# Kernel tuning notes

Hardware: AMD Instinct MI355X
Metric: run time of the kernel (lower is better)

The kernel has to match this reference:

```python
import jax, jax.numpy as jnp
import numpy as np

N, D, B, H = 131072, 512, 512, 8  # nodes, hidden_dim, graphs, heads


def setup_inputs() -> dict:
    key = jax.random.key(0)
    ks = jax.random.split(key, 4)
    x = jax.random.normal(ks[0], (N, D), jnp.float32)
    # sorted segment ids; every graph nonempty (matches torch batch.max()+1 semantics)
    batch = jnp.sort(jnp.arange(N, dtype=jnp.int32) % B)
    query = jax.random.normal(ks[1], (D,), jnp.float32)          # nn.Parameter(randn(1,1,D))
    W_in = jax.random.normal(ks[2], (3 * D, D), jnp.float32) / np.sqrt(D)  # MHA in_proj_weight
    b_in = jnp.zeros((3 * D,), jnp.float32)
    W_out = jax.random.normal(ks[3], (D, D), jnp.float32) / np.sqrt(D)     # MHA out_proj
    b_out = jnp.zeros((D,), jnp.float32)
    return {"x": x, "batch": batch, "num_graphs": B, "query": query,
            "W_in": W_in, "b_in": b_in, "W_out": W_out, "b_out": b_out}


def reference(x, batch, num_graphs, query, W_in, b_in, W_out, b_out):
    # Fused ragged single-query multihead attention pooling (eval mode: dropout off).
    D = x.shape[1]
    dh = D // H
    scale = 1.0 / np.sqrt(dh)
    # q/k/v projections (torch MHA packed in_proj: rows [0:D]=q, [D:2D]=k, [2D:3D]=v)
    q = ((query @ W_in[:D].T + b_in[:D]) * scale).reshape(H, dh)       # [H, dh], shared across graphs
    k = (x @ W_in[D:2 * D].T + b_in[D:2 * D]).reshape(-1, H, dh)       # [N, H, dh]
    v = (x @ W_in[2 * D:].T + b_in[2 * D:]).reshape(-1, H, dh)         # [N, H, dh]
    scores = jnp.einsum('nhd,hd->nh', k, q)                             # [N, H]
    # segment (per-graph) softmax over nodes
    smax = jax.ops.segment_max(scores, batch, num_segments=num_graphs)  # [B, H]
    e = jnp.exp(scores - smax[batch])
    denom = jax.ops.segment_sum(e, batch, num_segments=num_graphs)      # [B, H]
    p = e / denom[batch]                                                # [N, H]
    pooled = jax.ops.segment_sum(p[:, :, None] * v, batch, num_segments=num_graphs)  # [B, H, dh]
    return pooled.reshape(num_graphs, D) @ W_out.T + b_out              # [B, D]
```

## Files before the change

kernel.cpp:

```cpp
#include <hip/hip_runtime.h>
#include <math.h>

#define NHEAD 8

template <int CTRL>
__device__ __forceinline__ float dpp_add(float v) {
    int r = __builtin_amdgcn_mov_dpp(__float_as_int(v), CTRL, 0xF, 0xF, false);
    return v + __int_as_float(r);
}

__global__ void __launch_bounds__(256) k_setup(const float* __restrict__ query,
                                               const float* __restrict__ W_in,
                                               const float* __restrict__ b_in,
                                               const int* __restrict__ batch,
                                               float* __restrict__ wsc,
                                               int* __restrict__ seg_start,
                                               int* __restrict__ seg_end,
                                               int N, float scale) {
    const int g = blockIdx.x, t = threadIdx.x;
    if (g < 16) {
        __shared__ float qs4[64][4];
        __shared__ float qs[64];
        const int h = g >> 1, half = g & 1;
        {
            const int d = t & 63, qtr = t >> 6;
            const int row = h * 64 + d;
            const float4* wq = reinterpret_cast<const float4*>(W_in + (size_t)row * 512 + qtr * 128);
            const float4* qv = reinterpret_cast<const float4*>(query + qtr * 128);
            float a = 0.f;
#pragma unroll 8
            for (int i = 0; i < 32; ++i) {
                float4 w = wq[i], q = qv[i];
                a += w.x * q.x + w.y * q.y + w.z * q.z + w.w * q.w;
            }
            qs4[d][qtr] = a;
        }
        __syncthreads();
        if (t < 64) {
            const float s = qs4[t][0] + qs4[t][1] + qs4[t][2] + qs4[t][3];
            qs[t] = (s + b_in[h * 64 + t]) * scale;
        }
        __syncthreads();
        const int i = half * 256 + t;
        const float* Wk = W_in + (size_t)512 * 512;
        float a = 0.f;
#pragma unroll 8
        for (int d = 0; d < 64; ++d)
            a += qs[d] * Wk[(size_t)(h * 64 + d) * 512 + i];
        wsc[h * 512 + i] = a;
    } else {
        const int stride = (gridDim.x - 16) * 256;
        for (int n = (g - 16) * 256 + t; n < N; n += stride) {
            int b = batch[n];
            if (n == 0 || batch[n - 1] != b) seg_start[b] = n;
            if (n == N - 1 || batch[n + 1] != b) seg_end[b] = n + 1;
        }
    }
}

__global__ void __launch_bounds__(256) k_escore(const float* __restrict__ x,
                                                const float* __restrict__ wsc,
                                                float* __restrict__ e, int N) {
    const int t = threadIdx.x, lane = t & 63, wid = t >> 6;
    float4 w0[NHEAD], w1[NHEAD];
#pragma unroll
    for (int h = 0; h < NHEAD; ++h) {
        w0[h] = *reinterpret_cast<const float4*>(wsc + h * 512 + lane * 8);
        w1[h] = *reinterpret_cast<const float4*>(wsc + h * 512 + lane * 8 + 4);
    }
    const int base = (blockIdx.x * 4 + wid) * 16;
    if (base >= N) return;

    const float* xr0 = x + (size_t)base * 512 + lane * 8;
    float4 xa = *reinterpret_cast<const float4*>(xr0);
    float4 xb = *reinterpret_cast<const float4*>(xr0 + 4);

    for (int r = 0; r < 16; ++r) {
        const int row = base + r;
        if (row >= N) return;
        const float4 ca = xa, cb = xb;
        if (r + 1 < 16 && row + 1 < N) {
            const float* xr = x + (size_t)(row + 1) * 512 + lane * 8;
            xa = *reinterpret_cast<const float4*>(xr);
            xb = *reinterpret_cast<const float4*>(xr + 4);
        }
        float acc[NHEAD];
#pragma unroll
        for (int h = 0; h < NHEAD; ++h) {
            acc[h] = ca.x * w0[h].x + ca.y * w0[h].y + ca.z * w0[h].z + ca.w * w0[h].w +
                     cb.x * w1[h].x + cb.y * w1[h].y + cb.z * w1[h].z + cb.w * w1[h].w;
        }
#pragma unroll
        for (int h = 0; h < NHEAD; ++h) {
            float a = acc[h];
            a = dpp_add<0xB1>(a);
            a = dpp_add<0x4E>(a);
            a = dpp_add<0x141>(a);
            a = dpp_add<0x140>(a);
            a += __shfl_xor(a, 16, 64);
            a += __shfl_xor(a, 32, 64);
            acc[h] = __expf(a);
        }
        if (lane == 0) {
            float4 s0 = {acc[0], acc[1], acc[2], acc[3]};
            float4 s1 = {acc[4], acc[5], acc[6], acc[7]};
            float4* ep = reinterpret_cast<float4*>(e + (size_t)row * 8);
            ep[0] = s0;
            ep[1] = s1;
        }
    }
}

__global__ void __launch_bounds__(256) k_xp(const float* __restrict__ x,
                                            const float* __restrict__ e,
                                            const int* __restrict__ seg_start,
                                            const int* __restrict__ seg_end,
                                            float* __restrict__ xp) {
    const int b = gridDim.x - 1 - blockIdx.x;
    const int cc0 = blockIdx.y * 128;
    const int t = threadIdx.x;
    const int cl = t & 31, rg = t >> 5;
    __shared__ float p_lds[64][NHEAD];
    __shared__ float red[32][256];
    __shared__ float rl_lds[NHEAD];
    const int s0 = seg_start[b], s1 = seg_end[b];

    float acc[NHEAD][4];
#pragma unroll
    for (int h = 0; h < NHEAD; ++h)
#pragma unroll
        for (int k = 0; k < 4; ++k) acc[h][k] = 0.f;
    float lacc = 0.f;

    const int r0 = t >> 3, hh = t & 7;
    const int ntiles = (s1 - s0 + 63) >> 6;
    for (int ti = ntiles - 1; ti >= 0; --ti) {
        const int tbase = s0 + ti * 64;
        const int lim = min(64, s1 - tbase);
        p_lds[r0][hh] = (r0 < lim) ? e[(size_t)(tbase + r0) * 8 + hh] : 0.f;
        p_lds[r0 + 32][hh] = (r0 + 32 < lim) ? e[(size_t)(tbase + r0 + 32) * 8 + hh] : 0.f;
        __syncthreads();
        if (t < 64) {
            const int lh = t & 7, lrg = t >> 3;
#pragma unroll
            for (int j = 0; j < 8; ++j) lacc += p_lds[lrg * 8 + j][lh];
        }
        if (lim == 64) {
#pragma unroll
            for (int j = 0; j < 8; ++j) {
                const int r = rg + j * 8;
                const float4 xv = *reinterpret_cast<const float4*>(x + (size_t)(tbase + r) * 512 + cc0 + cl * 4);
                const float4 p0 = *reinterpret_cast<const float4*>(&p_lds[r][0]);
                const float4 p1 = *reinterpret_cast<const float4*>(&p_lds[r][4]);
                acc[0][0] += p0.x * xv.x; acc[0][1] += p0.x * xv.y; acc[0][2] += p0.x * xv.z; acc[0][3] += p0.x * xv.w;
                acc[1][0] += p0.y * xv.x; acc[1][1] += p0.y * xv.y; acc[1][2] += p0.y * xv.z; acc[1][3] += p0.y * xv.w;
                acc[2][0] += p0.z * xv.x; acc[2][1] += p0.z * xv.y; acc[2][2] += p0.z * xv.z; acc[2][3] += p0.z * xv.w;
                acc[3][0] += p0.w * xv.x; acc[3][1] += p0.w * xv.y; acc[3][2] += p0.w * xv.z; acc[3][3] += p0.w * xv.w;
                acc[4][0] += p1.x * xv.x; acc[4][1] += p1.x * xv.y; acc[4][2] += p1.x * xv.z; acc[4][3] += p1.x * xv.w;
                acc[5][0] += p1.y * xv.x; acc[5][1] += p1.y * xv.y; acc[5][2] += p1.y * xv.z; acc[5][3] += p1.y * xv.w;
                acc[6][0] += p1.z * xv.x; acc[6][1] += p1.z * xv.y; acc[6][2] += p1.z * xv.z; acc[6][3] += p1.z * xv.w;
                acc[7][0] += p1.w * xv.x; acc[7][1] += p1.w * xv.y; acc[7][2] += p1.w * xv.z; acc[7][3] += p1.w * xv.w;
            }
        } else {
            for (int r = rg; r < lim; r += 8) {
                const float4 xv = *reinterpret_cast<const float4*>(x + (size_t)(tbase + r) * 512 + cc0 + cl * 4);
                const float4 p0 = *reinterpret_cast<const float4*>(&p_lds[r][0]);
                const float4 p1 = *reinterpret_cast<const float4*>(&p_lds[r][4]);
                acc[0][0] += p0.x * xv.x; acc[0][1] += p0.x * xv.y; acc[0][2] += p0.x * xv.z; acc[0][3] += p0.x * xv.w;
                acc[1][0] += p0.y * xv.x; acc[1][1] += p0.y * xv.y; acc[1][2] += p0.y * xv.z; acc[1][3] += p0.y * xv.w;
                acc[2][0] += p0.z * xv.x; acc[2][1] += p0.z * xv.y; acc[2][2] += p0.z * xv.z; acc[2][3] += p0.z * xv.w;
                acc[3][0] += p0.w * xv.x; acc[3][1] += p0.w * xv.y; acc[3][2] += p0.w * xv.z; acc[3][3] += p0.w * xv.w;
                acc[4][0] += p1.x * xv.x; acc[4][1] += p1.x * xv.y; acc[4][2] += p1.x * xv.z; acc[4][3] += p1.x * xv.w;
                acc[5][0] += p1.y * xv.x; acc[5][1] += p1.y * xv.y; acc[5][2] += p1.y * xv.z; acc[5][3] += p1.y * xv.w;
                acc[6][0] += p1.z * xv.x; acc[6][1] += p1.z * xv.y; acc[6][2] += p1.z * xv.z; acc[6][3] += p1.z * xv.w;
                acc[7][0] += p1.w * xv.x; acc[7][1] += p1.w * xv.y; acc[7][2] += p1.w * xv.z; acc[7][3] += p1.w * xv.w;
            }
        }
        __syncthreads();
    }

    if (t < 64) {
        lacc += __shfl_xor(lacc, 8, 64);
        lacc += __shfl_xor(lacc, 16, 64);
        lacc += __shfl_xor(lacc, 32, 64);
        if (t < NHEAD) rl_lds[t] = 1.f / lacc;
    }
#pragma unroll
    for (int h = 0; h < NHEAD; ++h)
#pragma unroll
        for (int k = 0; k < 4; ++k) red[h * 4 + k][t] = acc[h][k];
    __syncthreads();
    {
        const int ho = t >> 5, cg = t & 31;
        const float rl = rl_lds[ho];
        float4 s = {0.f, 0.f, 0.f, 0.f};
#pragma unroll
        for (int g = 0; g < 8; ++g) {
            const int owner = g * 32 + cg;
            s.x += red[ho * 4 + 0][owner];
            s.y += red[ho * 4 + 1][owner];
            s.z += red[ho * 4 + 2][owner];
            s.w += red[ho * 4 + 3][owner];
        }
        s.x *= rl; s.y *= rl; s.z *= rl; s.w *= rl;
        *reinterpret_cast<float4*>(xp + (size_t)b * (NHEAD * 512) + (size_t)ho * 512 + cc0 + cg * 4) = s;
    }
}

__global__ void __launch_bounds__(256) k_gemm_tn4w(const float* __restrict__ A, int lda, int zA,
                                                   const float* __restrict__ Bm, int ldb, int zB,
                                                   const float* __restrict__ bias, int zBias,
                                                   float* __restrict__ C, int ldc, int zC, int K) {
    __shared__ float As[4][32][36];
    __shared__ float Bs[4][32][36];
    __shared__ float red[4][32][32];
    const int z = blockIdx.z;
    A += (size_t)z * zA;
    Bm += (size_t)z * zB;
    bias += (size_t)z * zBias;
    C += (size_t)z * zC;
    const int m0 = blockIdx.x * 32, n0 = blockIdx.y * 32;
    const int t = threadIdx.x;
    const int w = t >> 6, lane = t & 63;
    const int row = lane >> 1, c0 = (lane & 1) * 16;
    const int ty = lane >> 3, tx = lane & 7;
    const int Kw = K >> 2;
    const int kw0 = w * Kw;
    float c[4][4];
#pragma unroll
    for (int i = 0; i < 4; ++i)
#pragma unroll
        for (int j = 0; j < 4; ++j) c[i][j] = 0.f;

    for (int kt = 0; kt < Kw; kt += 32) {
        const int k0 = kw0 + kt;
        const float* Ar = A + (size_t)(m0 + row) * lda + k0 + c0;
        const float* Br = Bm + (size_t)(n0 + row) * ldb + k0 + c0;
        float4 a4[4], b4[4];
#pragma unroll
        for (int j = 0; j < 4; ++j) {
            a4[j] = *reinterpret_cast<const float4*>(Ar + j * 4);
            b4[j] = *reinterpret_cast<const float4*>(Br + j * 4);
        }
#pragma unroll
        for (int j = 0; j < 4; ++j) {
            As[w][c0 + j * 4 + 0][row] = a4[j].x;
            As[w][c0 + j * 4 + 1][row] = a4[j].y;
            As[w][c0 + j * 4 + 2][row] = a4[j].z;
            As[w][c0 + j * 4 + 3][row] = a4[j].w;
            Bs[w][c0 + j * 4 + 0][row] = b4[j].x;
            Bs[w][c0 + j * 4 + 1][row] = b4[j].y;
            Bs[w][c0 + j * 4 + 2][row] = b4[j].z;
            Bs[w][c0 + j * 4 + 3][row] = b4[j].w;
        }
#pragma unroll
        for (int kk = 0; kk < 32; ++kk) {
            float4 av = *reinterpret_cast<const float4*>(&As[w][kk][ty * 4]);
            float4 bv = *reinterpret_cast<const float4*>(&Bs[w][kk][tx * 4]);
            c[0][0] += av.x * bv.x; c[0][1] += av.x * bv.y; c[0][2] += av.x * bv.z; c[0][3] += av.x * bv.w;
            c[1][0] += av.y * bv.x; c[1][1] += av.y * bv.y; c[1][2] += av.y * bv.z; c[1][3] += av.y * bv.w;
            c[2][0] += av.z * bv.x; c[2][1] += av.z * bv.y; c[2][2] += av.z * bv.z; c[2][3] += av.z * bv.w;
            c[3][0] += av.w * bv.x; c[3][1] += av.w * bv.y; c[3][2] += av.w * bv.z; c[3][3] += av.w * bv.w;
        }
    }
#pragma unroll
    for (int i = 0; i < 4; ++i)
#pragma unroll
        for (int j = 0; j < 4; ++j) red[w][ty * 4 + i][tx * 4 + j] = c[i][j];
    __syncthreads();
    const int r = t >> 3, cc = (t & 7) * 4;
    float4 s = {0.f, 0.f, 0.f, 0.f};
#pragma unroll
    for (int g = 0; g < 4; ++g) {
        const float4 v = *reinterpret_cast<const float4*>(&red[g][r][cc]);
        s.x += v.x; s.y += v.y; s.z += v.z; s.w += v.w;
    }
    const float4 bv4 = *reinterpret_cast<const float4*>(bias + n0 + cc);
    float4 o = {s.x + bv4.x, s.y + bv4.y, s.z + bv4.z, s.w + bv4.w};
    *reinterpret_cast<float4*>(C + (size_t)(m0 + r) * ldc + n0 + cc) = o;
}

extern "C" void kernel_launch(void* const* d_in, const int* in_sizes, int n_in,
                              void* d_out, int out_size, void* d_ws, size_t ws_size,
                              hipStream_t stream) {
    const float* x     = (const float*)d_in[0];
    const int*   batch = (const int*)d_in[1];
    const float* query = (const float*)d_in[3];
    const float* W_in  = (const float*)d_in[4];
    const float* b_in  = (const float*)d_in[5];
    const float* W_out = (const float*)d_in[6];
    const float* b_out = (const float*)d_in[7];
    float* out = (float*)d_out;

    const int D = in_sizes[3];
    const int N = in_sizes[0] / D;
    const int B = out_size / D;
    const int dh = D / NHEAD;
    const float scale = 1.0f / sqrtf((float)dh);

    float* wsf       = (float*)d_ws;
    float* wsc       = wsf;
    float* e_ws      = wsc + NHEAD * 512;
    float* xp        = e_ws + (size_t)N * NHEAD;
    float* pooled    = xp + (size_t)B * NHEAD * 512;
    int*   seg_start = (int*)(pooled + (size_t)B * 512);
    int*   seg_end   = seg_start + B;

    k_setup<<<16 + 256, 256, 0, stream>>>(query, W_in, b_in, batch, wsc,
                                          seg_start, seg_end, N, scale);

    k_escore<<<(N + 63) / 64, 256, 0, stream>>>(x, wsc, e_ws, N);

    k_xp<<<dim3(B, 4), 256, 0, stream>>>(x, e_ws, seg_start, seg_end, xp);

    k_gemm_tn4w<<<dim3(B / 32, dh / 32, NHEAD), 256, 0, stream>>>(
        xp, NHEAD * 512, 512,
        W_in + (size_t)2 * D * D, D, dh * D,
        b_in + 2 * D, dh,
        pooled, D, dh, D);

    k_gemm_tn4w<<<dim3(B / 32, D / 32, 1), 256, 0, stream>>>(
        pooled, D, 0,
        W_out, D, 0,
        b_out, 0,
        out, D, 0, D);
}
```

Baseline: 127.4 us.

## Fuse score/exp and weighted pooling into one per-graph kernel

Replaces the separate score kernel and pooling kernel with one kernel per graph. Each wave streams its share of the graph's rows once, computes the exp-scores and accumulates the weighted sums of x and the denominators in registers, then merges the four waves through LDS. This avoids reading x twice and the round trip of the e buffer through memory. In exchange each block now holds 64 accumulators plus weights per thread, which raises register pressure, and only 512 blocks cover the whole input. There is still no max subtraction, matching the code before.

```diff
diff --git a/kernel.cpp b/kernel.cpp
--- a/kernel.cpp
+++ b/kernel.cpp
@@ -58,152 +58,108 @@
     }
 }
 
-__global__ void __launch_bounds__(256) k_escore(const float* __restrict__ x,
-                                                const float* __restrict__ wsc,
-                                                float* __restrict__ e, int N) {
-    const int t = threadIdx.x, lane = t & 63, wid = t >> 6;
+__global__ void __launch_bounds__(256, 2) k_fused1(const float* __restrict__ x,
+                                                   const float* __restrict__ wsc,
+                                                   const int* __restrict__ seg_start,
+                                                   const int* __restrict__ seg_end,
+                                                   float* __restrict__ xp) {
+    __shared__ float mrg[4][64][64];
+    __shared__ float dsum[4][NHEAD];
+    const int b = blockIdx.x, t = threadIdx.x;
+    const int lane = t & 63, w = t >> 6;
+    const int s0 = seg_start[b], s1 = seg_end[b];
+    const int len = s1 - s0;
+    const int clen = (len + 3) >> 2;
+    const int r0 = s0 + w * clen;
+    const int r1 = min(s1, r0 + clen);
+
     float4 w0[NHEAD], w1[NHEAD];
 #pragma unroll
     for (int h = 0; h < NHEAD; ++h) {
         w0[h] = *reinterpret_cast<const float4*>(wsc + h * 512 + lane * 8);
         w1[h] = *reinterpret_cast<const float4*>(wsc + h * 512 + lane * 8 + 4);
     }
-    const int base = (blockIdx.x * 4 + wid) * 16;
-    if (base >= N) return;
-
-    const float* xr0 = x + (size_t)base * 512 + lane * 8;
-    float4 xa = *reinterpret_cast<const float4*>(xr0);
-    float4 xb = *reinterpret_cast<const float4*>(xr0 + 4);
-
-    for (int r = 0; r < 16; ++r) {
-        const int row = base + r;
-        if (row >= N) return;
-        const float4 ca = xa, cb = xb;
-        if (r + 1 < 16 && row + 1 < N) {
-            const float* xr = x + (size_t)(row + 1) * 512 + lane * 8;
-            xa = *reinterpret_cast<const float4*>(xr);
-            xb = *reinterpret_cast<const float4*>(xr + 4);
-        }
-        float acc[NHEAD];
+
+    float acc[NHEAD][8];
+#pragma unroll
+    for (int h = 0; h < NHEAD; ++h)
+#pragma unroll
+        for (int j = 0; j < 8; ++j) acc[h][j] = 0.f;
+    float dacc[NHEAD];
+#pragma unroll
+    for (int h = 0; h < NHEAD; ++h) dacc[h] = 0.f;
+
+    float4 a0, a1, n0, n1;
+    const float* xl = x + lane * 8;
+    if (r0 < r1) {
+        a0 = *reinterpret_cast<const float4*>(xl + (size_t)r0 * 512);
+        a1 = *reinterpret_cast<const float4*>(xl + (size_t)r0 * 512 + 4);
+    }
+    if (r0 + 1 < r1) {
+        n0 = *reinterpret_cast<const float4*>(xl + (size_t)(r0 + 1) * 512);
+        n1 = *reinterpret_cast<const float4*>(xl + (size_t)(r0 + 1) * 512 + 4);
+    }
+
+    for (int r = r0; r < r1; ++r) {
+        const float4 c0 = a0, c1 = a1;
+        a0 = n0; a1 = n1;
+        if (r + 2 < r1) {
+            n0 = *reinterpret_cast<const float4*>(xl + (size_t)(r + 2) * 512);
+            n1 = *reinterpret_cast<const float4*>(xl + (size_t)(r + 2) * 512 + 4);
+        }
+        float e[NHEAD];
 #pragma unroll
         for (int h = 0; h < NHEAD; ++h) {
-            acc[h] = ca.x * w0[h].x + ca.y * w0[h].y + ca.z * w0[h].z + ca.w * w0[h].w +
-                     cb.x * w1[h].x + cb.y * w1[h].y + cb.z * w1[h].z + cb.w * w1[h].w;
+            float d = c0.x * w0[h].x + c0.y * w0[h].y + c0.z * w0[h].z + c0.w * w0[h].w +
+                      c1.x * w1[h].x + c1.y * w1[h].y + c1.z * w1[h].z + c1.w * w1[h].w;
+            d = dpp_add<0xB1>(d);
+            d = dpp_add<0x4E>(d);
+            d = dpp_add<0x141>(d);
+            d = dpp_add<0x140>(d);
+            d += __shfl_xor(d, 16, 64);
+            d += __shfl_xor(d, 32, 64);
+            e[h] = __expf(d);
         }
 #pragma unroll
         for (int h = 0; h < NHEAD; ++h) {
-            float a = acc[h];
-            a = dpp_add<0xB1>(a);
-            a = dpp_add<0x4E>(a);
-            a = dpp_add<0x141>(a);
-            a = dpp_add<0x140>(a);
-            a += __shfl_xor(a, 16, 64);
-            a += __shfl_xor(a, 32, 64);
-            acc[h] = __expf(a);
-        }
-        if (lane == 0) {
-            float4 s0 = {acc[0], acc[1], acc[2], acc[3]};
-            float4 s1 = {acc[4], acc[5], acc[6], acc[7]};
-            float4* ep = reinterpret_cast<float4*>(e + (size_t)row * 8);
-            ep[0] = s0;
-            ep[1] = s1;
-        }
-    }
-}
-
-__global__ void __launch_bounds__(256) k_xp(const float* __restrict__ x,
-                                            const float* __restrict__ e,
-                                            const int* __restrict__ seg_start,
-                                            const int* __restrict__ seg_end,
-                                            float* __restrict__ xp) {
-    const int b = gridDim.x - 1 - blockIdx.x;
-    const int cc0 = blockIdx.y * 128;
-    const int t = threadIdx.x;
-    const int cl = t & 31, rg = t >> 5;
-    __shared__ float p_lds[64][NHEAD];
-    __shared__ float red[32][256];
-    __shared__ float rl_lds[NHEAD];
-    const int s0 = seg_start[b], s1 = seg_end[b];
-
-    float acc[NHEAD][4];
+            dacc[h] += e[h];
+            acc[h][0] += e[h] * c0.x; acc[h][1] += e[h] * c0.y;
+            acc[h][2] += e[h] * c0.z; acc[h][3] += e[h] * c0.w;
+            acc[h][4] += e[h] * c1.x; acc[h][5] += e[h] * c1.y;
+            acc[h][6] += e[h] * c1.z; acc[h][7] += e[h] * c1.w;
+        }
+    }
+
 #pragma unroll
     for (int h = 0; h < NHEAD; ++h)
 #pragma unroll
-        for (int k = 0; k < 4; ++k) acc[h][k] = 0.f;
-    float lacc = 0.f;
-
-    const int r0 = t >> 3, hh = t & 7;
-    const int ntiles = (s1 - s0 + 63) >> 6;
-    for (int ti = ntiles - 1; ti >= 0; --ti) {
-        const int tbase = s0 + ti * 64;
-        const int lim = min(64, s1 - tbase);
-        p_lds[r0][hh] = (r0 < lim) ? e[(size_t)(tbase + r0) * 8 + hh] : 0.f;
-        p_lds[r0 + 32][hh] = (r0 + 32 < lim) ? e[(size_t)(tbase + r0 + 32) * 8 + hh] : 0.f;
-        __syncthreads();
-        if (t < 64) {
-            const int lh = t & 7, lrg = t >> 3;
-#pragma unroll
-            for (int j = 0; j < 8; ++j) lacc += p_lds[lrg * 8 + j][lh];
-        }
-        if (lim == 64) {
-#pragma unroll
-            for (int j = 0; j < 8; ++j) {
-                const int r = rg + j * 8;
-                const float4 xv = *reinterpret_cast<const float4*>(x + (size_t)(tbase + r) * 512 + cc0 + cl * 4);
-                const float4 p0 = *reinterpret_cast<const float4*>(&p_lds[r][0]);
-                const float4 p1 = *reinterpret_cast<const float4*>(&p_lds[r][4]);
-                acc[0][0] += p0.x * xv.x; acc[0][1] += p0.x * xv.y; acc[0][2] += p0.x * xv.z; acc[0][3] += p0.x * xv.w;
-                acc[1][0] += p0.y * xv.x; acc[1][1] += p0.y * xv.y; acc[1][2] += p0.y * xv.z; acc[1][3] += p0.y * xv.w;
-                acc[2][0] += p0.z * xv.x; acc[2][1] += p0.z * xv.y; acc[2][2] += p0.z * xv.z; acc[2][3] += p0.z * xv.w;
-                acc[3][0] += p0.w * xv.x; acc[3][1] += p0.w * xv.y; acc[3][2] += p0.w * xv.z; acc[3][3] += p0.w * xv.w;
-                acc[4][0] += p1.x * xv.x; acc[4][1] += p1.x * xv.y; acc[4][2] += p1.x * xv.z; acc[4][3] += p1.x * xv.w;
-                acc[5][0] += p1.y * xv.x; acc[5][1] += p1.y * xv.y; acc[5][2] += p1.y * xv.z; acc[5][3] += p1.y * xv.w;
-                acc[6][0] += p1.z * xv.x; acc[6][1] += p1.z * xv.y; acc[6][2] += p1.z * xv.z; acc[6][3] += p1.z * xv.w;
-                acc[7][0] += p1.w * xv.x; acc[7][1] += p1.w * xv.y; acc[7][2] += p1.w * xv.z; acc[7][3] += p1.w * xv.w;
+        for (int j = 0; j < 8; ++j)
+            mrg[w][h * 8 + j][lane] = acc[h][j];
+    if (lane == 0) {
+#pragma unroll
+        for (int h = 0; h < NHEAD; ++h) dsum[w][h] = dacc[h];
+    }
+    __syncthreads();
+
+    {
+        const int c0i = 2 * t;
+        const int lsrc = c0i >> 3, slot = c0i & 7;
+        float* xpb = xp + (size_t)b * (NHEAD * 512);
+#pragma unroll
+        for (int h = 0; h < NHEAD; ++h) {
+            const float den = dsum[0][h] + dsum[1][h] + dsum[2][h] + dsum[3][h];
+            const float rl = 1.f / den;
+            float num0 = 0.f, num1 = 0.f;
+#pragma unroll
+            for (int g = 0; g < 4; ++g) {
+                num0 += mrg[g][h * 8 + slot][lsrc];
+                num1 += mrg[g][h * 8 + slot + 1][lsrc];
             }
-        } else {
-            for (int r = rg; r < lim; r += 8) {
-                const float4 xv = *reinterpret_cast<const float4*>(x + (size_t)(tbase + r) * 512 + cc0 + cl * 4);
-                const float4 p0 = *reinterpret_cast<const float4*>(&p_lds[r][0]);
-                const float4 p1 = *reinterpret_cast<const float4*>(&p_lds[r][4]);
-                acc[0][0] += p0.x * xv.x; acc[0][1] += p0.x * xv.y; acc[0][2] += p0.x * xv.z; acc[0][3] += p0.x * xv.w;
-                acc[1][0] += p0.y * xv.x; acc[1][1] += p0.y * xv.y; acc[1][2] += p0.y * xv.z; acc[1][3] += p0.y * xv.w;
-                acc[2][0] += p0.z * xv.x; acc[2][1] += p0.z * xv.y; acc[2][2] += p0.z * xv.z; acc[2][3] += p0.z * xv.w;
-                acc[3][0] += p0.w * xv.x; acc[3][1] += p0.w * xv.y; acc[3][2] += p0.w * xv.z; acc[3][3] += p0.w * xv.w;
-                acc[4][0] += p1.x * xv.x; acc[4][1] += p1.x * xv.y; acc[4][2] += p1.x * xv.z; acc[4][3] += p1.x * xv.w;
-                acc[5][0] += p1.y * xv.x; acc[5][1] += p1.y * xv.y; acc[5][2] += p1.y * xv.z; acc[5][3] += p1.y * xv.w;
-                acc[6][0] += p1.z * xv.x; acc[6][1] += p1.z * xv.y; acc[6][2] += p1.z * xv.z; acc[6][3] += p1.z * xv.w;
-                acc[7][0] += p1.w * xv.x; acc[7][1] += p1.w * xv.y; acc[7][2] += p1.w * xv.z; acc[7][3] += p1.w * xv.w;
-            }
-        }
-        __syncthreads();
-    }
-
-    if (t < 64) {
-        lacc += __shfl_xor(lacc, 8, 64);
-        lacc += __shfl_xor(lacc, 16, 64);
-        lacc += __shfl_xor(lacc, 32, 64);
-        if (t < NHEAD) rl_lds[t] = 1.f / lacc;
-    }
-#pragma unroll
-    for (int h = 0; h < NHEAD; ++h)
-#pragma unroll
-        for (int k = 0; k < 4; ++k) red[h * 4 + k][t] = acc[h][k];
-    __syncthreads();
-    {
-        const int ho = t >> 5, cg = t & 31;
-        const float rl = rl_lds[ho];
-        float4 s = {0.f, 0.f, 0.f, 0.f};
-#pragma unroll
-        for (int g = 0; g < 8; ++g) {
-            const int owner = g * 32 + cg;
-            s.x += red[ho * 4 + 0][owner];
-            s.y += red[ho * 4 + 1][owner];
-            s.z += red[ho * 4 + 2][owner];
-            s.w += red[ho * 4 + 3][owner];
-        }
-        s.x *= rl; s.y *= rl; s.z *= rl; s.w *= rl;
-        *reinterpret_cast<float4*>(xp + (size_t)b * (NHEAD * 512) + (size_t)ho * 512 + cc0 + cg * 4) = s;
+            float2 o;
+            o.x = num0 * rl;
+            o.y = num1 * rl;
+            *reinterpret_cast<float2*>(xpb + (size_t)h * 512 + c0i) = o;
+        }
     }
 }
 
@@ -300,8 +256,7 @@
 
     float* wsf       = (float*)d_ws;
     float* wsc       = wsf;
-    float* e_ws      = wsc + NHEAD * 512;
-    float* xp        = e_ws + (size_t)N * NHEAD;
+    float* xp        = wsc + NHEAD * 512;
     float* pooled    = xp + (size_t)B * NHEAD * 512;
     int*   seg_start = (int*)(pooled + (size_t)B * 512);
     int*   seg_end   = seg_start + B;
@@ -309,9 +264,7 @@
     k_setup<<<16 + 256, 256, 0, stream>>>(query, W_in, b_in, batch, wsc,
                                           seg_start, seg_end, N, scale);
 
-    k_escore<<<(N + 63) / 64, 256, 0, stream>>>(x, wsc, e_ws, N);
-
-    k_xp<<<dim3(B, 4), 256, 0, stream>>>(x, e_ws, seg_start, seg_end, xp);
+    k_fused1<<<B, 256, 0, stream>>>(x, wsc, seg_start, seg_end, xp);
 
     k_gemm_tn4w<<<dim3(B / 32, dh / 32, NHEAD), 256, 0, stream>>>(
         xp, NHEAD * 512, 512,
```

Result: faster. 105.5 us (-17.2%).
